# Optimization experiments

Measured on AMD Instinct MI355X. Metric: run time of the kernel, lower is better.

The kernel has to match this reference:

```python
import jax, jax.numpy as jnp
import numpy as np

NU = 100000   # num user nodes
NI = 100000   # num item nodes
E = 200000    # edges per edge type
C = 256       # channels
L = 2         # num layers
EPS = 1e-5


def _ln(x, g, b):
    mu = jnp.mean(x, axis=-1, keepdims=True)
    xc = x - mu
    var = jnp.mean(xc * xc, axis=-1, keepdims=True)
    return xc * jax.lax.rsqrt(var + EPS) * g + b


def _prmp_conv(x_src, x_dst, ei, pw1, pb1, pw2, pb2, mg, mb, lw, lb):
    # ei: [2, E] with row0 = source node idx, row1 = destination node idx
    src, dst = ei[0], ei[1]
    # prediction MLP on detached destination (parent) features, gathered per edge
    xi = jax.lax.stop_gradient(x_dst)[dst]              # [E, C]
    predicted = jax.nn.relu(xi @ pw1 + pb1) @ pw2 + pb2  # [E, C]
    residual = x_src[src] - predicted                    # [E, C]
    msg = _ln(residual, mg, mb)                          # LayerNorm over channels
    n_dst = x_dst.shape[0]
    agg = jax.ops.segment_sum(msg, dst, num_segments=n_dst)
    cnt = jax.ops.segment_sum(jnp.ones((ei.shape[1],), msg.dtype), dst, num_segments=n_dst)
    agg = agg / jnp.maximum(cnt, 1.0)[:, None]           # mean aggregation
    # GraphSAGE-style update: concat(dst, aggregated residuals) -> linear
    return jnp.concatenate([x_dst, agg], axis=-1) @ lw + lb


def setup_inputs() -> dict:
    key = jax.random.key(0)
    ks = jax.random.split(key, 14)
    s1 = 1.0 / np.sqrt(C)
    s2 = 1.0 / np.sqrt(2 * C)
    return {
        "x_user": jax.random.normal(ks[0], (NU, C), jnp.float32),
        "x_item": jax.random.normal(ks[1], (NI, C), jnp.float32),
        "pw1": jax.random.normal(ks[2], (L, 2, C, C), jnp.float32) * s1,
        "pb1": jax.random.normal(ks[3], (L, 2, C), jnp.float32) * 0.01,
        "pw2": jax.random.normal(ks[4], (L, 2, C, C), jnp.float32) * s1,
        "pb2": jax.random.normal(ks[5], (L, 2, C), jnp.float32) * 0.01,
        "msg_g": jnp.ones((L, 2, C), jnp.float32),
        "msg_b": jnp.zeros((L, 2, C), jnp.float32),
        "lin_w": jax.random.normal(ks[6], (L, 2, 2 * C, C), jnp.float32) * s2,
        "lin_b": jax.random.normal(ks[7], (L, 2, C), jnp.float32) * 0.01,
        "node_g": jnp.ones((L, 2, C), jnp.float32),
        "node_b": jnp.zeros((L, 2, C), jnp.float32),
        "ei_ui": jax.random.randint(ks[8], (2, E), 0, NU, jnp.int32),  # user -> item
        "ei_iu": jax.random.randint(ks[9], (2, E), 0, NI, jnp.int32),  # item -> user
    }


def reference(x_user, x_item, pw1, pb1, pw2, pb2, msg_g, msg_b, lin_w, lin_b,
              node_g, node_b, ei_ui, ei_iu):
    xu, xi = x_user, x_item
    for l in range(L):
        # edge type 0: user -> item (dst = item); edge type 1: item -> user (dst = user)
        new_i = _prmp_conv(xu, xi, ei_ui, pw1[l, 0], pb1[l, 0], pw2[l, 0], pb2[l, 0],
                           msg_g[l, 0], msg_b[l, 0], lin_w[l, 0], lin_b[l, 0])
        new_u = _prmp_conv(xi, xu, ei_iu, pw1[l, 1], pb1[l, 1], pw2[l, 1], pb2[l, 1],
                           msg_g[l, 1], msg_b[l, 1], lin_w[l, 1], lin_b[l, 1])
        # per-node-type LayerNorm (mode='node') + relu; node_type 0 = user, 1 = item
        xu = jax.nn.relu(_ln(new_u, node_g[l, 0], node_b[l, 0]))
        xi = jax.nn.relu(_ln(new_i, node_g[l, 1], node_b[l, 1]))
    return jnp.concatenate([xu, xi], axis=0)  # [NU + NI, C]
```

## Files before the change

kernel.cpp:

```cpp
#include <hip/hip_runtime.h>
#include <cstddef>
#include <cstdint>

#define CCH 256

typedef unsigned short ushort_t;
typedef short bf16x8 __attribute__((ext_vector_type(8)));
typedef float f32x4 __attribute__((ext_vector_type(4)));

__device__ __forceinline__ ushort_t f2bf(float f) {
    unsigned u = __float_as_uint(f);
    u = u + 0x7FFFu + ((u >> 16) & 1u);
    return (ushort_t)(u >> 16);
}
__device__ __forceinline__ float bf2f(ushort_t h) {
    return __uint_as_float(((unsigned)h) << 16);
}

__device__ __forceinline__ void gload16(const void* g, void* l) {
    __builtin_amdgcn_global_load_lds((const __attribute__((address_space(1))) unsigned*)g,
                                     (__attribute__((address_space(3))) unsigned*)l, 16, 0, 0);
}

template<int EPI>
__global__ __launch_bounds__(512)
void gemm_kernel(const ushort_t* __restrict__ A0, const ushort_t* __restrict__ A1,
                 int M, int K,
                 const ushort_t* __restrict__ BT,
                 const float* __restrict__ bias,
                 const float* __restrict__ lng, const float* __restrict__ lnb,
                 float* __restrict__ outF, ushort_t* __restrict__ outB)
{
    __shared__ ushort_t As[128 * 32];
    __shared__ ushort_t Bs[256 * 32];
    const int tid = threadIdx.x;
    const int w  = tid >> 6, l = tid & 63;
    const int ln = l & 15,  kh = l >> 4;
    const int m0 = blockIdx.x * 128;

    const int  arow = w * 16 + (l >> 2);
    const long arg  = min((long)(m0 + arow), (long)(M - 1));
    const int  asl  = (l & 3) * 8;
    ushort_t* aDst = As + w * 512;
    const int  brow = w * 32 + (l >> 2);
    const int  bsl  = (l & 3) * 8;
    ushort_t* bDst0 = Bs + w * 1024;
    ushort_t* bDst1 = Bs + w * 1024 + 512;

    f32x4 acc[16];
    #pragma unroll
    for (int i = 0; i < 16; ++i) acc[i] = (f32x4)0.f;

    for (int kc = 0; kc < K; kc += 32) {
        const ushort_t* Asel = (kc < 256) ? A0 : A1;
        gload16(Asel + arg * 256 + (kc & 255) + asl, aDst);
        gload16(BT + (long)brow * K + kc + bsl, bDst0);
        gload16(BT + (long)(brow + 16) * K + kc + bsl, bDst1);
        __syncthreads();
        const bf16x8 af = *(const bf16x8*)&As[(w * 16 + ln) * 32 + kh * 8];
        #pragma unroll
        for (int fn = 0; fn < 16; ++fn) {
            const bf16x8 bf = *(const bf16x8*)&Bs[(fn * 16 + ln) * 32 + kh * 8];
            acc[fn] = __builtin_amdgcn_mfma_f32_16x16x32_bf16(af, bf, acc[fn], 0, 0, 0);
        }
        __syncthreads();
    }

    if (EPI <= 1) {
        #pragma unroll
        for (int fn = 0; fn < 16; ++fn) {
            const int col = fn * 16 + ln;
            const float bv = bias[col];
            #pragma unroll
            for (int j = 0; j < 4; ++j) {
                const long gr = m0 + w * 16 + kh * 4 + j;
                float v = acc[fn][j] + bv;
                if (EPI == 0) v = fmaxf(v, 0.f);
                if (gr < M) outB[gr * 256 + col] = f2bf(v);
            }
        }
    } else {
        #pragma unroll
        for (int fn = 0; fn < 16; ++fn) {
            const float bv = bias[fn * 16 + ln];
            #pragma unroll
            for (int j = 0; j < 4; ++j) acc[fn][j] += bv;
        }
        #pragma unroll
        for (int j = 0; j < 4; ++j) {
            float s = 0.f, q = 0.f;
            #pragma unroll
            for (int fn = 0; fn < 16; ++fn) { const float v = acc[fn][j]; s += v; q += v * v; }
            #pragma unroll
            for (int m = 1; m < 16; m <<= 1) { s += __shfl_xor(s, m); q += __shfl_xor(q, m); }
            const float mu   = s * (1.f / 256.f);
            const float var  = q * (1.f / 256.f) - mu * mu;
            const float rstd = rsqrtf(var + 1e-5f);
            const long gr = m0 + w * 16 + kh * 4 + j;
            if (gr < M) {
                #pragma unroll
                for (int fn = 0; fn < 16; ++fn) {
                    const int col = fn * 16 + ln;
                    float y = (acc[fn][j] - mu) * rstd * lng[col] + lnb[col];
                    y = fmaxf(y, 0.f);
                    outF[gr * 256 + col] = y;
                    outB[gr * 256 + col] = f2bf(y);
                }
            }
        }
    }
}

__global__ __launch_bounds__(256)
void edge_kernel(const float* __restrict__ xsrc,
                 const ushort_t* __restrict__ P,
                 const int* __restrict__ ei, int E,
                 const float* __restrict__ mg, const float* __restrict__ mb,
                 float* __restrict__ agg)
{
    __shared__ float xp[4][256];
    const int tid = threadIdx.x;
    const int wv = tid >> 6, l = tid & 63;
    const int c4 = l * 4;
    const float4 mgv = *(const float4*)&mg[c4];
    const float4 mbv = *(const float4*)&mb[c4];
    const int base = (blockIdx.x * 4 + wv) * 8;
    for (int it = 0; it < 8; ++it) {
        const int e = base + it;
        const bool ok = (e < E);
        int d = 0;
        float r0 = 0.f, r1 = 0.f, r2 = 0.f, r3 = 0.f;
        if (ok) {
            const int s = ei[e];
            d = ei[E + e];
            const float4  xs = *(const float4*)&xsrc[(size_t)s * 256 + c4];
            const ushort4 pv = *(const ushort4*)&P[(size_t)d * 256 + c4];
            r0 = xs.x - bf2f(pv.x); r1 = xs.y - bf2f(pv.y);
            r2 = xs.z - bf2f(pv.z); r3 = xs.w - bf2f(pv.w);
        }
        float sm = r0 + r1 + r2 + r3;
        float sq = r0 * r0 + r1 * r1 + r2 * r2 + r3 * r3;
        #pragma unroll
        for (int m = 32; m >= 1; m >>= 1) { sm += __shfl_xor(sm, m); sq += __shfl_xor(sq, m); }
        const float mu   = sm * (1.f / 256.f);
        const float var  = sq * (1.f / 256.f) - mu * mu;
        const float rstd = rsqrtf(var + 1e-5f);
        float4 msg;
        msg.x = (r0 - mu) * rstd * mgv.x + mbv.x;
        msg.y = (r1 - mu) * rstd * mgv.y + mbv.y;
        msg.z = (r2 - mu) * rstd * mgv.z + mbv.z;
        msg.w = (r3 - mu) * rstd * mgv.w + mbv.w;
        *(float4*)&xp[wv][c4] = msg;
        __syncthreads();
        if (ok) {
            float* ap = agg + (size_t)d * 256;
            atomicAdd(ap + l,       xp[wv][l]);
            atomicAdd(ap + l + 64,  xp[wv][l + 64]);
            atomicAdd(ap + l + 128, xp[wv][l + 128]);
            atomicAdd(ap + l + 192, xp[wv][l + 192]);
        }
        __syncthreads();
    }
}

__global__ void conv_bf_kernel(const float* __restrict__ in, ushort_t* __restrict__ out, long n4)
{
    long i = (long)blockIdx.x * blockDim.x + threadIdx.x;
    const long stride = (long)gridDim.x * blockDim.x;
    for (; i < n4; i += stride) {
        const float4 v = ((const float4*)in)[i];
        ushort4 o; o.x = f2bf(v.x); o.y = f2bf(v.y); o.z = f2bf(v.z); o.w = f2bf(v.w);
        ((ushort4*)out)[i] = o;
    }
}

__global__ void div_bf_kernel(const float* __restrict__ agg, const float* __restrict__ cnt,
                              int N, ushort_t* __restrict__ out)
{
    long i = (long)blockIdx.x * blockDim.x + threadIdx.x;
    const long n4 = (long)N * 64;
    const long stride = (long)gridDim.x * blockDim.x;
    for (; i < n4; i += stride) {
        const float4 v = ((const float4*)agg)[i];
        const float inv = 1.f / fmaxf(cnt[i >> 6], 1.f);
        ushort4 o;
        o.x = f2bf(v.x * inv); o.y = f2bf(v.y * inv);
        o.z = f2bf(v.z * inv); o.w = f2bf(v.w * inv);
        ((ushort4*)out)[i] = o;
    }
}

__global__ void count_kernel(const int* __restrict__ ei, int E, float* __restrict__ cnt)
{
    const int i = blockIdx.x * blockDim.x + threadIdx.x;
    if (i < E) atomicAdd(&cnt[ei[E + i]], 1.f);
}

__global__ void transpose_w_kernel(const float* __restrict__ in, ushort_t* __restrict__ out,
                                   int K, int N)
{
    __shared__ float t[32][33];
    const int b  = blockIdx.z;
    const int k0 = blockIdx.x * 32, n0 = blockIdx.y * 32;
    const int tx = threadIdx.x, ty = threadIdx.y;
    const float* src = in + (size_t)b * K * N;
    #pragma unroll
    for (int j = 0; j < 32; j += 8) t[ty + j][tx] = src[(size_t)(k0 + ty + j) * N + n0 + tx];
    __syncthreads();
    ushort_t* dst = out + (size_t)b * N * K;
    #pragma unroll
    for (int j = 0; j < 32; j += 8) dst[(size_t)(n0 + ty + j) * K + k0 + tx] = f2bf(t[tx][ty + j]);
}

extern "C" void kernel_launch(void* const* d_in, const int* in_sizes, int n_in,
                              void* d_out, int out_size, void* d_ws, size_t ws_size,
                              hipStream_t stream)
{
    const float* x_user = (const float*)d_in[0];
    const float* x_item = (const float*)d_in[1];
    const float* pw1    = (const float*)d_in[2];
    const float* pb1    = (const float*)d_in[3];
    const float* pw2    = (const float*)d_in[4];
    const float* pb2    = (const float*)d_in[5];
    const float* msg_g  = (const float*)d_in[6];
    const float* msg_b  = (const float*)d_in[7];
    const float* lin_w  = (const float*)d_in[8];
    const float* lin_b  = (const float*)d_in[9];
    const float* node_g = (const float*)d_in[10];
    const float* node_b = (const float*)d_in[11];
    const int*   ei_ui  = (const int*)d_in[12];
    const int*   ei_iu  = (const int*)d_in[13];

    const int NU = in_sizes[0] / CCH;
    const int NI = in_sizes[1] / CCH;
    const int E0 = in_sizes[12] / 2;
    const int E1 = in_sizes[13] / 2;
    const int L  = in_sizes[2] / (2 * CCH * CCH);
    const long Nmax = (NU > NI) ? NU : NI;

    float* agg_i = (float*)d_ws;
    float* agg_u = agg_i + (size_t)NI * CCH;
    float* cnt_i = agg_u + (size_t)NU * CCH;
    float* cnt_u = cnt_i + NI;
    ushort_t* Xu_bf = (ushort_t*)(cnt_u + NU);
    ushort_t* Xi_bf = Xu_bf + (size_t)NU * CCH;
    ushort_t* Hbf   = Xi_bf + (size_t)NI * CCH;
    ushort_t* Pbf   = Hbf + Nmax * CCH;
    ushort_t* pw1T  = Pbf + Nmax * CCH;
    ushort_t* pw2T  = pw1T + (size_t)L * 2 * CCH * CCH;
    ushort_t* linT  = pw2T + (size_t)L * 2 * CCH * CCH;

    float* Xu_f = (float*)d_out;
    float* Xi_f = Xu_f + (size_t)NU * CCH;

    hipMemsetAsync(cnt_i, 0, (size_t)(NI + NU) * sizeof(float), stream);
    count_kernel<<<(E0 + 255) / 256, 256, 0, stream>>>(ei_ui, E0, cnt_i);
    count_kernel<<<(E1 + 255) / 256, 256, 0, stream>>>(ei_iu, E1, cnt_u);
    conv_bf_kernel<<<2048, 256, 0, stream>>>(x_user, Xu_bf, (long)NU * 64);
    conv_bf_kernel<<<2048, 256, 0, stream>>>(x_item, Xi_bf, (long)NI * 64);
    {
        dim3 b(32, 8);
        transpose_w_kernel<<<dim3(8, 8, L * 2), b, 0, stream>>>(pw1, pw1T, 256, 256);
        transpose_w_kernel<<<dim3(8, 8, L * 2), b, 0, stream>>>(pw2, pw2T, 256, 256);
        transpose_w_kernel<<<dim3(16, 8, L * 2), b, 0, stream>>>(lin_w, linT, 512, 256);
    }

    const int gI = (NI + 127) / 128, gU = (NU + 127) / 128;

    for (int l = 0; l < L; ++l) {
        hipMemsetAsync(agg_i, 0, (size_t)(NI + NU) * CCH * sizeof(float), stream);

        const size_t pw0 = ((size_t)l * 2 + 0) * CCH * CCH;
        const size_t pw1o = ((size_t)l * 2 + 1) * CCH * CCH;
        const size_t b0  = ((size_t)l * 2 + 0) * CCH;
        const size_t b1  = ((size_t)l * 2 + 1) * CCH;
        const size_t lw0 = ((size_t)l * 2 + 0) * 2 * CCH * CCH;
        const size_t lw1 = ((size_t)l * 2 + 1) * 2 * CCH * CCH;

        const float* xu_cur = (l == 0) ? x_user : Xu_f;
        const float* xi_cur = (l == 0) ? x_item : Xi_f;

        gemm_kernel<0><<<gI, 512, 0, stream>>>(Xi_bf, nullptr, NI, 256, pw1T + pw0,
                                               pb1 + b0, nullptr, nullptr, nullptr, Hbf);
        gemm_kernel<1><<<gI, 512, 0, stream>>>(Hbf, nullptr, NI, 256, pw2T + pw0,
                                               pb2 + b0, nullptr, nullptr, nullptr, Pbf);
        edge_kernel<<<(E0 + 31) / 32, 256, 0, stream>>>(xu_cur, Pbf, ei_ui, E0,
                                                        msg_g + b0, msg_b + b0, agg_i);

        gemm_kernel<0><<<gU, 512, 0, stream>>>(Xu_bf, nullptr, NU, 256, pw1T + pw1o,
                                               pb1 + b1, nullptr, nullptr, nullptr, Hbf);
        gemm_kernel<1><<<gU, 512, 0, stream>>>(Hbf, nullptr, NU, 256, pw2T + pw1o,
                                               pb2 + b1, nullptr, nullptr, nullptr, Pbf);
        edge_kernel<<<(E1 + 31) / 32, 256, 0, stream>>>(xi_cur, Pbf, ei_iu, E1,
                                                        msg_g + b1, msg_b + b1, agg_u);

        div_bf_kernel<<<2048, 256, 0, stream>>>(agg_i, cnt_i, NI, Hbf);
        div_bf_kernel<<<2048, 256, 0, stream>>>(agg_u, cnt_u, NU, Pbf);

        gemm_kernel<2><<<gI, 512, 0, stream>>>(Xi_bf, Hbf, NI, 512, linT + lw0,
                                               lin_b + b0, node_g + b1, node_b + b1,
                                               Xi_f, Xi_bf);
        gemm_kernel<2><<<gU, 512, 0, stream>>>(Xu_bf, Pbf, NU, 512, linT + lw1,
                                               lin_b + b1, node_g + b0, node_b + b0,
                                               Xu_f, Xu_bf);
    }
}
```

Before: 2.005 ms.

## Aggregate edge messages in packed fp16 atomics and retile GEMMs with swizzled LDS

The edge kernel now reads bf16 source features, divides each message by the destination degree up front, and accumulates into an fp16 buffer with packed v2f16 atomics. The separate divide/convert pass goes away, because the final linear GEMM consumes the fp16 aggregate directly through f16 MFMA on its second K half, with the matching weights stored as fp16. The GEMMs are retiled: 256-thread blocks, 128x128 tiles split over N for the prediction MLP, 64x256 tiles with a cross-wave LayerNorm reduction for the update, and an XOR swizzle on LDS to avoid bank conflicts. The goal is to halve atomic and memset traffic and cut kernel count, at the cost of fp16 accumulation precision and possible overflow or rounding error in the aggregates.

```diff
diff --git a/kernel.cpp b/kernel.cpp
--- a/kernel.cpp
+++ b/kernel.cpp
@@ -1,11 +1,13 @@
 #include <hip/hip_runtime.h>
+#include <hip/hip_fp16.h>
 #include <cstddef>
-#include <cstdint>
 
 #define CCH 256
 
 typedef unsigned short ushort_t;
 typedef short bf16x8 __attribute__((ext_vector_type(8)));
+typedef _Float16 f16x8 __attribute__((ext_vector_type(8)));
+typedef _Float16 f16x2 __attribute__((ext_vector_type(2)));
 typedef float f32x4 __attribute__((ext_vector_type(4)));
 
 __device__ __forceinline__ ushort_t f2bf(float f) {
@@ -16,14 +18,28 @@
 __device__ __forceinline__ float bf2f(ushort_t h) {
     return __uint_as_float(((unsigned)h) << 16);
 }
+__device__ __forceinline__ ushort_t f2h(float f) {
+    _Float16 h = (_Float16)f;
+    return __builtin_bit_cast(unsigned short, h);
+}
 
 __device__ __forceinline__ void gload16(const void* g, void* l) {
     __builtin_amdgcn_global_load_lds((const __attribute__((address_space(1))) unsigned*)g,
                                      (__attribute__((address_space(3))) unsigned*)l, 16, 0, 0);
 }
 
+__device__ __forceinline__ void atomic_add_f16x2(void* p, float a, float b) {
+    f16x2 v; v[0] = (_Float16)a; v[1] = (_Float16)b;
+#if __has_builtin(__builtin_amdgcn_global_atomic_fadd_v2f16)
+    (void)__builtin_amdgcn_global_atomic_fadd_v2f16(
+        (__attribute__((address_space(1))) f16x2*)p, v);
+#else
+    (void)unsafeAtomicAdd((__half2*)p, *(__half2*)&v);
+#endif
+}
+
 template<int EPI>
-__global__ __launch_bounds__(512)
+__global__ __launch_bounds__(256)
 void gemm_kernel(const ushort_t* __restrict__ A0, const ushort_t* __restrict__ A1,
                  int M, int K,
                  const ushort_t* __restrict__ BT,
@@ -31,136 +47,185 @@
                  const float* __restrict__ lng, const float* __restrict__ lnb,
                  float* __restrict__ outF, ushort_t* __restrict__ outB)
 {
-    __shared__ ushort_t As[128 * 32];
-    __shared__ ushort_t Bs[256 * 32];
+    constexpr int BM = (EPI == 2) ? 64 : 128;
+    constexpr int BN = (EPI == 2) ? 256 : 128;
+    __shared__ __align__(16) ushort_t As[BM * 32];
+    __shared__ __align__(16) ushort_t Bs[BN * 32];
+    __shared__ float lnp[(EPI == 2) ? 64 : 1][8];
+
     const int tid = threadIdx.x;
-    const int w  = tid >> 6, l = tid & 63;
-    const int ln = l & 15,  kh = l >> 4;
-    const int m0 = blockIdx.x * 128;
-
-    const int  arow = w * 16 + (l >> 2);
-    const long arg  = min((long)(m0 + arow), (long)(M - 1));
-    const int  asl  = (l & 3) * 8;
-    ushort_t* aDst = As + w * 512;
-    const int  brow = w * 32 + (l >> 2);
-    const int  bsl  = (l & 3) * 8;
-    ushort_t* bDst0 = Bs + w * 1024;
-    ushort_t* bDst1 = Bs + w * 1024 + 512;
-
-    f32x4 acc[16];
+    const int w = tid >> 6, l = tid & 63;
+    const int ln = l & 15, kh = l >> 4;
+    const int wr = (EPI == 2) ? 0 : (w >> 1);
+    const int wc = (EPI == 2) ? w : (w & 1);
+    const int m0 = blockIdx.x * BM;
+    const int n0 = (EPI == 2) ? 0 : (blockIdx.y * BN);
+
+    const int gsl = ((l & 3) ^ ((l >> 3) & 3)) << 3;
+    const int sw8 = (kh ^ ((ln >> 1) & 3)) << 3;
+
+    f32x4 acc[4][4];
     #pragma unroll
-    for (int i = 0; i < 16; ++i) acc[i] = (f32x4)0.f;
+    for (int m = 0; m < 4; ++m)
+        #pragma unroll
+        for (int n = 0; n < 4; ++n) acc[m][n] = (f32x4)0.f;
 
     for (int kc = 0; kc < K; kc += 32) {
-        const ushort_t* Asel = (kc < 256) ? A0 : A1;
-        gload16(Asel + arg * 256 + (kc & 255) + asl, aDst);
-        gload16(BT + (long)brow * K + kc + bsl, bDst0);
-        gload16(BT + (long)(brow + 16) * K + kc + bsl, bDst1);
+        const ushort_t* Ap = A0;
+        if constexpr (EPI == 2) { if (kc >= 256) Ap = A1; }
+        #pragma unroll
+        for (int i = 0; i < BM / 64; ++i) {
+            const int rl = w * (BM / 4) + i * 16 + (l >> 2);
+            long gr = m0 + rl; if (gr > M - 1) gr = M - 1;
+            gload16(Ap + gr * 256 + (kc & 255) + gsl,
+                    (void*)(As + w * (BM / 4) * 32 + i * 512));
+        }
+        #pragma unroll
+        for (int i = 0; i < BN / 64; ++i) {
+            const int rl = w * (BN / 4) + i * 16 + (l >> 2);
+            gload16(BT + (long)(n0 + rl) * K + kc + gsl,
+                    (void*)(Bs + w * (BN / 4) * 32 + i * 512));
+        }
         __syncthreads();
-        const bf16x8 af = *(const bf16x8*)&As[(w * 16 + ln) * 32 + kh * 8];
-        #pragma unroll
-        for (int fn = 0; fn < 16; ++fn) {
-            const bf16x8 bf = *(const bf16x8*)&Bs[(fn * 16 + ln) * 32 + kh * 8];
-            acc[fn] = __builtin_amdgcn_mfma_f32_16x16x32_bf16(af, bf, acc[fn], 0, 0, 0);
+
+        bf16x8 afr[4], bfr[4];
+        #pragma unroll
+        for (int m = 0; m < 4; ++m)
+            afr[m] = *(const bf16x8*)&As[(wr * 64 + m * 16 + ln) * 32 + sw8];
+        #pragma unroll
+        for (int n = 0; n < 4; ++n)
+            bfr[n] = *(const bf16x8*)&Bs[(wc * 64 + n * 16 + ln) * 32 + sw8];
+
+        bool use_f16 = false;
+        if constexpr (EPI == 2) use_f16 = (kc >= 256);
+        if (use_f16) {
+            #pragma unroll
+            for (int m = 0; m < 4; ++m)
+                #pragma unroll
+                for (int n = 0; n < 4; ++n)
+                    acc[m][n] = __builtin_amdgcn_mfma_f32_16x16x32_f16(
+                        __builtin_bit_cast(f16x8, afr[m]),
+                        __builtin_bit_cast(f16x8, bfr[n]), acc[m][n], 0, 0, 0);
+        } else {
+            #pragma unroll
+            for (int m = 0; m < 4; ++m)
+                #pragma unroll
+                for (int n = 0; n < 4; ++n)
+                    acc[m][n] = __builtin_amdgcn_mfma_f32_16x16x32_bf16(
+                        afr[m], bfr[n], acc[m][n], 0, 0, 0);
         }
         __syncthreads();
     }
 
-    if (EPI <= 1) {
-        #pragma unroll
-        for (int fn = 0; fn < 16; ++fn) {
-            const int col = fn * 16 + ln;
+    if constexpr (EPI <= 1) {
+        #pragma unroll
+        for (int n = 0; n < 4; ++n) {
+            const int col = n0 + wc * 64 + n * 16 + ln;
             const float bv = bias[col];
             #pragma unroll
+            for (int m = 0; m < 4; ++m)
+                #pragma unroll
+                for (int j = 0; j < 4; ++j) {
+                    const long gr = m0 + wr * 64 + m * 16 + kh * 4 + j;
+                    float v = acc[m][n][j] + bv;
+                    if (EPI == 0) v = fmaxf(v, 0.f);
+                    if (gr < M) outB[gr * 256 + col] = f2bf(v);
+                }
+        }
+    } else {
+        float gv[4], bv2[4];
+        #pragma unroll
+        for (int n = 0; n < 4; ++n) {
+            const int col = wc * 64 + n * 16 + ln;
+            const float bv = bias[col];
+            gv[n] = lng[col]; bv2[n] = lnb[col];
+            #pragma unroll
+            for (int m = 0; m < 4; ++m)
+                #pragma unroll
+                for (int j = 0; j < 4; ++j) acc[m][n][j] += bv;
+        }
+        #pragma unroll
+        for (int m = 0; m < 4; ++m)
+            #pragma unroll
             for (int j = 0; j < 4; ++j) {
-                const long gr = m0 + w * 16 + kh * 4 + j;
-                float v = acc[fn][j] + bv;
-                if (EPI == 0) v = fmaxf(v, 0.f);
-                if (gr < M) outB[gr * 256 + col] = f2bf(v);
-            }
-        }
-    } else {
-        #pragma unroll
-        for (int fn = 0; fn < 16; ++fn) {
-            const float bv = bias[fn * 16 + ln];
-            #pragma unroll
-            for (int j = 0; j < 4; ++j) acc[fn][j] += bv;
-        }
-        #pragma unroll
-        for (int j = 0; j < 4; ++j) {
-            float s = 0.f, q = 0.f;
-            #pragma unroll
-            for (int fn = 0; fn < 16; ++fn) { const float v = acc[fn][j]; s += v; q += v * v; }
-            #pragma unroll
-            for (int m = 1; m < 16; m <<= 1) { s += __shfl_xor(s, m); q += __shfl_xor(q, m); }
-            const float mu   = s * (1.f / 256.f);
-            const float var  = q * (1.f / 256.f) - mu * mu;
-            const float rstd = rsqrtf(var + 1e-5f);
-            const long gr = m0 + w * 16 + kh * 4 + j;
-            if (gr < M) {
-                #pragma unroll
-                for (int fn = 0; fn < 16; ++fn) {
-                    const int col = fn * 16 + ln;
-                    float y = (acc[fn][j] - mu) * rstd * lng[col] + lnb[col];
-                    y = fmaxf(y, 0.f);
-                    outF[gr * 256 + col] = y;
-                    outB[gr * 256 + col] = f2bf(y);
+                float s = 0.f, q = 0.f;
+                #pragma unroll
+                for (int n = 0; n < 4; ++n) { const float v = acc[m][n][j]; s += v; q += v * v; }
+                #pragma unroll
+                for (int mm = 1; mm < 16; mm <<= 1) { s += __shfl_xor(s, mm); q += __shfl_xor(q, mm); }
+                if (ln == 0) {
+                    const int r = m * 16 + kh * 4 + j;
+                    lnp[r][wc] = s; lnp[r][4 + wc] = q;
                 }
             }
-        }
+        __syncthreads();
+        #pragma unroll
+        for (int m = 0; m < 4; ++m)
+            #pragma unroll
+            for (int j = 0; j < 4; ++j) {
+                const int r = m * 16 + kh * 4 + j;
+                const float4 s4 = *(const float4*)&lnp[r][0];
+                const float4 q4 = *(const float4*)&lnp[r][4];
+                const float s = s4.x + s4.y + s4.z + s4.w;
+                const float q = q4.x + q4.y + q4.z + q4.w;
+                const float mu = s * (1.f / 256.f);
+                const float var = q * (1.f / 256.f) - mu * mu;
+                const float rstd = rsqrtf(var + 1e-5f);
+                const long gr = m0 + r;
+                if (gr < M) {
+                    #pragma unroll
+                    for (int n = 0; n < 4; ++n) {
+                        const int col = wc * 64 + n * 16 + ln;
+                        float y = (acc[m][n][j] - mu) * rstd * gv[n] + bv2[n];
+                        y = fmaxf(y, 0.f);
+                        outF[gr * 256 + col] = y;
+                        outB[gr * 256 + col] = f2bf(y);
+                    }
+                }
+            }
     }
 }
 
 __global__ __launch_bounds__(256)
-void edge_kernel(const float* __restrict__ xsrc,
+void edge_kernel(const ushort_t* __restrict__ xsrc,
                  const ushort_t* __restrict__ P,
                  const int* __restrict__ ei, int E,
                  const float* __restrict__ mg, const float* __restrict__ mb,
-                 float* __restrict__ agg)
-{
-    __shared__ float xp[4][256];
-    const int tid = threadIdx.x;
-    const int wv = tid >> 6, l = tid & 63;
-    const int c4 = l * 4;
-    const float4 mgv = *(const float4*)&mg[c4];
-    const float4 mbv = *(const float4*)&mb[c4];
-    const int base = (blockIdx.x * 4 + wv) * 8;
-    for (int it = 0; it < 8; ++it) {
-        const int e = base + it;
-        const bool ok = (e < E);
-        int d = 0;
-        float r0 = 0.f, r1 = 0.f, r2 = 0.f, r3 = 0.f;
-        if (ok) {
-            const int s = ei[e];
-            d = ei[E + e];
-            const float4  xs = *(const float4*)&xsrc[(size_t)s * 256 + c4];
-            const ushort4 pv = *(const ushort4*)&P[(size_t)d * 256 + c4];
-            r0 = xs.x - bf2f(pv.x); r1 = xs.y - bf2f(pv.y);
-            r2 = xs.z - bf2f(pv.z); r3 = xs.w - bf2f(pv.w);
-        }
-        float sm = r0 + r1 + r2 + r3;
-        float sq = r0 * r0 + r1 * r1 + r2 * r2 + r3 * r3;
-        #pragma unroll
-        for (int m = 32; m >= 1; m >>= 1) { sm += __shfl_xor(sm, m); sq += __shfl_xor(sq, m); }
-        const float mu   = sm * (1.f / 256.f);
-        const float var  = sq * (1.f / 256.f) - mu * mu;
-        const float rstd = rsqrtf(var + 1e-5f);
-        float4 msg;
-        msg.x = (r0 - mu) * rstd * mgv.x + mbv.x;
-        msg.y = (r1 - mu) * rstd * mgv.y + mbv.y;
-        msg.z = (r2 - mu) * rstd * mgv.z + mbv.z;
-        msg.w = (r3 - mu) * rstd * mgv.w + mbv.w;
-        *(float4*)&xp[wv][c4] = msg;
-        __syncthreads();
-        if (ok) {
-            float* ap = agg + (size_t)d * 256;
-            atomicAdd(ap + l,       xp[wv][l]);
-            atomicAdd(ap + l + 64,  xp[wv][l + 64]);
-            atomicAdd(ap + l + 128, xp[wv][l + 128]);
-            atomicAdd(ap + l + 192, xp[wv][l + 192]);
-        }
-        __syncthreads();
-    }
+                 const float* __restrict__ cnt,
+                 unsigned* __restrict__ agg)
+{
+    const int l = threadIdx.x & 63;
+    const long e = (long)blockIdx.x * 4 + (threadIdx.x >> 6);
+    if (e >= E) return;
+    const int s = ei[e];
+    const int d = ei[E + e];
+    const float inv = 1.f / fmaxf(cnt[d], 1.f);
+    const unsigned xl = *(const unsigned*)&xsrc[(size_t)s * 256 + 2 * l];
+    const unsigned xh = *(const unsigned*)&xsrc[(size_t)s * 256 + 128 + 2 * l];
+    const unsigned pl = *(const unsigned*)&P[(size_t)d * 256 + 2 * l];
+    const unsigned ph = *(const unsigned*)&P[(size_t)d * 256 + 128 + 2 * l];
+    const float r0 = bf2f((ushort_t)(xl & 0xffff)) - bf2f((ushort_t)(pl & 0xffff));
+    const float r1 = bf2f((ushort_t)(xl >> 16))    - bf2f((ushort_t)(pl >> 16));
+    const float r2 = bf2f((ushort_t)(xh & 0xffff)) - bf2f((ushort_t)(ph & 0xffff));
+    const float r3 = bf2f((ushort_t)(xh >> 16))    - bf2f((ushort_t)(ph >> 16));
+    float sm = r0 + r1 + r2 + r3;
+    float sq = r0 * r0 + r1 * r1 + r2 * r2 + r3 * r3;
+    #pragma unroll
+    for (int m = 32; m >= 1; m >>= 1) { sm += __shfl_xor(sm, m); sq += __shfl_xor(sq, m); }
+    const float mu = sm * (1.f / 256.f);
+    const float var = sq * (1.f / 256.f) - mu * mu;
+    const float rstd = rsqrtf(var + 1e-5f);
+    const float2 g_lo = *(const float2*)&mg[2 * l];
+    const float2 g_hi = *(const float2*)&mg[128 + 2 * l];
+    const float2 b_lo = *(const float2*)&mb[2 * l];
+    const float2 b_hi = *(const float2*)&mb[128 + 2 * l];
+    const float m0v = ((r0 - mu) * rstd * g_lo.x + b_lo.x) * inv;
+    const float m1v = ((r1 - mu) * rstd * g_lo.y + b_lo.y) * inv;
+    const float m2v = ((r2 - mu) * rstd * g_hi.x + b_hi.x) * inv;
+    const float m3v = ((r3 - mu) * rstd * g_hi.y + b_hi.y) * inv;
+    unsigned* base = agg + (size_t)d * 128;
+    atomic_add_f16x2((void*)(base + l), m0v, m1v);
+    atomic_add_f16x2((void*)(base + 64 + l), m2v, m3v);
 }
 
 __global__ void conv_bf_kernel(const float* __restrict__ in, ushort_t* __restrict__ out, long n4)
@@ -174,22 +239,6 @@
     }
 }
 
-__global__ void div_bf_kernel(const float* __restrict__ agg, const float* __restrict__ cnt,
-                              int N, ushort_t* __restrict__ out)
-{
-    long i = (long)blockIdx.x * blockDim.x + threadIdx.x;
-    const long n4 = (long)N * 64;
-    const long stride = (long)gridDim.x * blockDim.x;
-    for (; i < n4; i += stride) {
-        const float4 v = ((const float4*)agg)[i];
-        const float inv = 1.f / fmaxf(cnt[i >> 6], 1.f);
-        ushort4 o;
-        o.x = f2bf(v.x * inv); o.y = f2bf(v.y * inv);
-        o.z = f2bf(v.z * inv); o.w = f2bf(v.w * inv);
-        ((ushort4*)out)[i] = o;
-    }
-}
-
 __global__ void count_kernel(const int* __restrict__ ei, int E, float* __restrict__ cnt)
 {
     const int i = blockIdx.x * blockDim.x + threadIdx.x;
@@ -197,10 +246,10 @@
 }
 
 __global__ void transpose_w_kernel(const float* __restrict__ in, ushort_t* __restrict__ out,
-                                   int K, int N)
+                                   int K, int N, int f16_from)
 {
     __shared__ float t[32][33];
-    const int b  = blockIdx.z;
+    const int b = blockIdx.z;
     const int k0 = blockIdx.x * 32, n0 = blockIdx.y * 32;
     const int tx = threadIdx.x, ty = threadIdx.y;
     const float* src = in + (size_t)b * K * N;
@@ -209,7 +258,11 @@
     __syncthreads();
     ushort_t* dst = out + (size_t)b * N * K;
     #pragma unroll
-    for (int j = 0; j < 32; j += 8) dst[(size_t)(n0 + ty + j) * K + k0 + tx] = f2bf(t[tx][ty + j]);
+    for (int j = 0; j < 32; j += 8) {
+        const float v = t[tx][ty + j];
+        const int kk = k0 + tx;
+        dst[(size_t)(n0 + ty + j) * K + kk] = (kk >= f16_from) ? f2h(v) : f2bf(v);
+    }
 }
 
 extern "C" void kernel_launch(void* const* d_in, const int* in_sizes, int n_in,
@@ -238,17 +291,18 @@
     const int L  = in_sizes[2] / (2 * CCH * CCH);
     const long Nmax = (NU > NI) ? NU : NI;
 
-    float* agg_i = (float*)d_ws;
-    float* agg_u = agg_i + (size_t)NI * CCH;
-    float* cnt_i = agg_u + (size_t)NU * CCH;
-    float* cnt_u = cnt_i + NI;
-    ushort_t* Xu_bf = (ushort_t*)(cnt_u + NU);
+    ushort_t* base  = (ushort_t*)d_ws;
+    ushort_t* agg_i = base;
+    ushort_t* agg_u = agg_i + (size_t)NI * CCH;
+    ushort_t* Xu_bf = agg_u + (size_t)NU * CCH;
     ushort_t* Xi_bf = Xu_bf + (size_t)NU * CCH;
     ushort_t* Hbf   = Xi_bf + (size_t)NI * CCH;
     ushort_t* Pbf   = Hbf + Nmax * CCH;
     ushort_t* pw1T  = Pbf + Nmax * CCH;
     ushort_t* pw2T  = pw1T + (size_t)L * 2 * CCH * CCH;
     ushort_t* linT  = pw2T + (size_t)L * 2 * CCH * CCH;
+    float*    cnt_i = (float*)(linT + (size_t)L * 2 * CCH * 2 * CCH);
+    float*    cnt_u = cnt_i + NI;
 
     float* Xu_f = (float*)d_out;
     float* Xi_f = Xu_f + (size_t)NU * CCH;
@@ -260,48 +314,45 @@
     conv_bf_kernel<<<2048, 256, 0, stream>>>(x_item, Xi_bf, (long)NI * 64);
     {
         dim3 b(32, 8);
-        transpose_w_kernel<<<dim3(8, 8, L * 2), b, 0, stream>>>(pw1, pw1T, 256, 256);
-        transpose_w_kernel<<<dim3(8, 8, L * 2), b, 0, stream>>>(pw2, pw2T, 256, 256);
-        transpose_w_kernel<<<dim3(16, 8, L * 2), b, 0, stream>>>(lin_w, linT, 512, 256);
-    }
-
-    const int gI = (NI + 127) / 128, gU = (NU + 127) / 128;
+        transpose_w_kernel<<<dim3(8, 8, L * 2), b, 0, stream>>>(pw1, pw1T, 256, 256, 1 << 30);
+        transpose_w_kernel<<<dim3(8, 8, L * 2), b, 0, stream>>>(pw2, pw2T, 256, 256, 1 << 30);
+        transpose_w_kernel<<<dim3(16, 8, L * 2), b, 0, stream>>>(lin_w, linT, 512, 256, 256);
+    }
+
+    const dim3 gS_I((NI + 127) / 128, 2), gS_U((NU + 127) / 128, 2);
+    const int  gL_I = (NI + 63) / 64,     gL_U = (NU + 63) / 64;
 
     for (int l = 0; l < L; ++l) {
-        hipMemsetAsync(agg_i, 0, (size_t)(NI + NU) * CCH * sizeof(float), stream);
-
-        const size_t pw0 = ((size_t)l * 2 + 0) * CCH * CCH;
-        const size_t pw1o = ((size_t)l * 2 + 1) * CCH * CCH;
+        hipMemsetAsync(agg_i, 0, (size_t)(NI + NU) * CCH * sizeof(ushort_t), stream);
+
+        const size_t w0  = ((size_t)l * 2 + 0) * CCH * CCH;
+        const size_t w1  = ((size_t)l * 2 + 1) * CCH * CCH;
         const size_t b0  = ((size_t)l * 2 + 0) * CCH;
         const size_t b1  = ((size_t)l * 2 + 1) * CCH;
         const size_t lw0 = ((size_t)l * 2 + 0) * 2 * CCH * CCH;
         const size_t lw1 = ((size_t)l * 2 + 1) * 2 * CCH * CCH;
 
-        const float* xu_cur = (l == 0) ? x_user : Xu_f;
-        const float* xi_cur = (l == 0) ? x_item : Xi_f;
-
-        gemm_kernel<0><<<gI, 512, 0, stream>>>(Xi_bf, nullptr, NI, 256, pw1T + pw0,
-                                               pb1 + b0, nullptr, nullptr, nullptr, Hbf);
-        gemm_kernel<1><<<gI, 512, 0, stream>>>(Hbf, nullptr, NI, 256, pw2T + pw0,
-                                               pb2 + b0, nullptr, nullptr, nullptr, Pbf);
-        edge_kernel<<<(E0 + 31) / 32, 256, 0, stream>>>(xu_cur, Pbf, ei_ui, E0,
-                                                        msg_g + b0, msg_b + b0, agg_i);
-
-        gemm_kernel<0><<<gU, 512, 0, stream>>>(Xu_bf, nullptr, NU, 256, pw1T + pw1o,
-                                               pb1 + b1, nullptr, nullptr, nullptr, Hbf);
-        gemm_kernel<1><<<gU, 512, 0, stream>>>(Hbf, nullptr, NU, 256, pw2T + pw1o,
-                                               pb2 + b1, nullptr, nullptr, nullptr, Pbf);
-        edge_kernel<<<(E1 + 31) / 32, 256, 0, stream>>>(xi_cur, Pbf, ei_iu, E1,
-                                                        msg_g + b1, msg_b + b1, agg_u);
-
-        div_bf_kernel<<<2048, 256, 0, stream>>>(agg_i, cnt_i, NI, Hbf);
-        div_bf_kernel<<<2048, 256, 0, stream>>>(agg_u, cnt_u, NU, Pbf);
-
-        gemm_kernel<2><<<gI, 512, 0, stream>>>(Xi_bf, Hbf, NI, 512, linT + lw0,
-                                               lin_b + b0, node_g + b1, node_b + b1,
-                                               Xi_f, Xi_bf);
-        gemm_kernel<2><<<gU, 512, 0, stream>>>(Xu_bf, Pbf, NU, 512, linT + lw1,
-                                               lin_b + b1, node_g + b0, node_b + b0,
-                                               Xu_f, Xu_bf);
-    }
-}
+        gemm_kernel<0><<<gS_I, 256, 0, stream>>>(Xi_bf, nullptr, NI, 256, pw1T + w0,
+                                                 pb1 + b0, nullptr, nullptr, nullptr, Hbf);
+        gemm_kernel<1><<<gS_I, 256, 0, stream>>>(Hbf, nullptr, NI, 256, pw2T + w0,
+                                                 pb2 + b0, nullptr, nullptr, nullptr, Pbf);
+        edge_kernel<<<(E0 + 3) / 4, 256, 0, stream>>>(Xu_bf, Pbf, ei_ui, E0,
+                                                      msg_g + b0, msg_b + b0, cnt_i,
+                                                      (unsigned*)agg_i);
+
+        gemm_kernel<0><<<gS_U, 256, 0, stream>>>(Xu_bf, nullptr, NU, 256, pw1T + w1,
+                                                 pb1 + b1, nullptr, nullptr, nullptr, Hbf);
+        gemm_kernel<1><<<gS_U, 256, 0, stream>>>(Hbf, nullptr, NU, 256, pw2T + w1,
+                                                 pb2 + b1, nullptr, nullptr, nullptr, Pbf);
+        edge_kernel<<<(E1 + 3) / 4, 256, 0, stream>>>(Xi_bf, Pbf, ei_iu, E1,
+                                                      msg_g + b1, msg_b + b1, cnt_u,
+                                                      (unsigned*)agg_u);
+
+        gemm_kernel<2><<<gL_I, 256, 0, stream>>>(Xi_bf, agg_i, NI, 512, linT + lw0,
+                                                 lin_b + b0, node_g + b1, node_b + b1,
+                                                 Xi_f, Xi_bf);
+        gemm_kernel<2><<<gL_U, 256, 0, stream>>>(Xu_bf, agg_u, NU, 512, linT + lw1,
+                                                 lin_b + b1, node_g + b0, node_b + b0,
+                                                 Xu_f, Xu_bf);
+    }
+}
```

Result: faster. 1.702 ms (-15.1%).
